# Optimization experiments

Measured on AMD Instinct MI355X. Metric: run time of the kernel, lower is better.

The kernel has to match this reference:

```python
import jax, jax.numpy as jnp
import numpy as np

E = 8        # n_routed_experts
Z = 4        # zero_expert_num (identity experts)
K = 2        # moe_topk
SCALE = 2.5  # routed_scaling_factor
T, H, I = 8192, 1024, 512


def setup_inputs() -> dict:
    key = jax.random.key(0)
    k0, k1, k2, k3, k4 = jax.random.split(key, 5)
    return {
        "hidden_states": jax.random.normal(k0, (T, H), jnp.float32),
        "router_w": jax.random.normal(k1, (E + Z, H), jnp.float32) * 0.02,
        "correction_bias": jax.random.normal(k2, (E + Z,), jnp.float32) * 0.01,
        "w13": jax.random.normal(k3, (E, 2 * I, H), jnp.float32) * 0.02,
        "w2": jax.random.normal(k4, (E, H, I), jnp.float32) * 0.02,
    }


def reference(hidden_states, router_w, correction_bias, w13, w2):
    # ---- router (float32) ----
    logits = hidden_states.astype(jnp.float32) @ router_w.T          # [T, E+Z]
    scores = jax.nn.softmax(logits, axis=-1)
    # correction bias only affects expert *selection*, not the gate weights
    _, topk_idx = jax.lax.top_k(scores + correction_bias, K)          # [T, K]
    topk_w = jnp.take_along_axis(scores, topk_idx, axis=-1)          # renormalize=False

    # ---- zero experts (identity type): idx >= E contributes scale * x ----
    is_zero = topk_idx >= E                                           # [T, K]
    routed_w = jnp.where(is_zero, 0.0, topk_w)
    zero_scale = jnp.where(is_zero, topk_w, 0.0).sum(-1, keepdims=True)
    zero_result = zero_scale * hidden_states                          # [T, H]

    # ---- combine weights per routed expert: [T, E] ----
    tok = jnp.arange(hidden_states.shape[0])[:, None]
    safe_idx = jnp.clip(topk_idx, 0, E - 1)   # zero-expert slots carry weight 0
    combine = jnp.zeros((hidden_states.shape[0], E), scores.dtype)
    combine = combine.at[tok, safe_idx].add(routed_w)

    # ---- grouped expert GEMMs (SiLU gated MLP), combined densely ----
    h = jnp.einsum('th,eih->eti', hidden_states, w13)                 # [E, T, 2I]
    g, u = jnp.split(h, 2, axis=-1)
    act = jax.nn.silu(g) * u                                          # [E, T, I]
    eo = jnp.einsum('eti,ehi->eth', act, w2)                          # [E, T, H]
    routed = jnp.einsum('te,eth->th', combine, eo)                    # [T, H]

    return routed * SCALE + zero_result
```

## Files before the change

kernel.cpp:

```cpp
#include <hip/hip_runtime.h>
#include <hip/hip_bf16.h>
#include <math.h>

typedef __bf16 bf16_t;
typedef bf16_t bf16x8 __attribute__((ext_vector_type(8)));
typedef float f32x4 __attribute__((ext_vector_type(4)));

#define T_TOK 8192
#define HDIM  1024
#define IDIM  512
#define NEXP  8
#define NTOT  12
#define MAXROWS (2 * T_TOK + NEXP * 128)
#define MAX_MTILES (MAXROWS / 128)

__device__ __forceinline__ void gll16(const bf16_t* g, bf16_t* l) {
  __builtin_amdgcn_global_load_lds((__attribute__((address_space(1))) void*)g,
                                   (__attribute__((address_space(3))) void*)l,
                                   16, 0, 0);
}

__global__ void cast_bf16_kernel(const float* __restrict__ in, bf16_t* __restrict__ out,
                                 size_t n8) {
  size_t gid = (size_t)blockIdx.x * blockDim.x + threadIdx.x;
  if (gid >= n8) return;
  size_t i = gid * 8;
  float4 a = *(const float4*)&in[i];
  float4 b = *(const float4*)&in[i + 4];
  bf16x8 o;
  o[0] = (bf16_t)a.x; o[1] = (bf16_t)a.y; o[2] = (bf16_t)a.z; o[3] = (bf16_t)a.w;
  o[4] = (bf16_t)b.x; o[5] = (bf16_t)b.y; o[6] = (bf16_t)b.z; o[7] = (bf16_t)b.w;
  *(bf16x8*)&out[i] = o;
}

__global__ void router_kernel(const float* __restrict__ x, const float* __restrict__ rw,
                              const float* __restrict__ bias,
                              int* __restrict__ tk_e, float* __restrict__ tk_w,
                              float* __restrict__ zscale) {
  int t = blockIdx.x;
  int l = threadIdx.x;
  const float4* xr = (const float4*)(x + (size_t)t * HDIM);
  float4 xv[4];
#pragma unroll
  for (int i = 0; i < 4; i++) xv[i] = xr[l + 64 * i];
  float part[NTOT];
#pragma unroll
  for (int e = 0; e < NTOT; e++) {
    const float4* wr = (const float4*)(rw + (size_t)e * HDIM);
    float s = 0.f;
#pragma unroll
    for (int i = 0; i < 4; i++) {
      float4 w = wr[l + 64 * i];
      s += xv[i].x * w.x + xv[i].y * w.y + xv[i].z * w.z + xv[i].w * w.w;
    }
    part[e] = s;
  }
#pragma unroll
  for (int off = 32; off > 0; off >>= 1)
#pragma unroll
    for (int e = 0; e < NTOT; e++) part[e] += __shfl_down(part[e], off);

  if (l == 0) {
    float mx = part[0];
#pragma unroll
    for (int e = 1; e < NTOT; e++) mx = fmaxf(mx, part[e]);
    float p[NTOT], den = 0.f;
#pragma unroll
    for (int e = 0; e < NTOT; e++) { p[e] = expf(part[e] - mx); den += p[e]; }
    float inv = 1.f / den;
#pragma unroll
    for (int e = 0; e < NTOT; e++) p[e] *= inv;
    float s0 = -1e30f, s1 = -1e30f; int i0 = 0, i1 = 0;
#pragma unroll
    for (int e = 0; e < NTOT; e++) {
      float v = p[e] + bias[e];
      if (v > s0) { s1 = s0; i1 = i0; s0 = v; i0 = e; }
      else if (v > s1) { s1 = v; i1 = e; }
    }
    float zs = 0.f;
    int idx[2] = { i0, i1 };
#pragma unroll
    for (int k = 0; k < 2; k++) {
      int e = idx[k];
      float w = p[e];
      if (e >= NEXP) { zs += w; tk_e[2 * t + k] = -1; tk_w[2 * t + k] = 0.f; }
      else           { tk_e[2 * t + k] = e; tk_w[2 * t + k] = w; }
    }
    zscale[t] = zs;
  }
}

__global__ void zero_init_kernel(int* __restrict__ counts, int* __restrict__ sel_tok,
                                 float* __restrict__ sel_w) {
  int i = blockIdx.x * blockDim.x + threadIdx.x;
  if (i < MAXROWS) { sel_tok[i] = 0; sel_w[i] = 0.f; }
  if (i < NEXP) counts[i] = 0;
}

__global__ void count_kernel(const int* __restrict__ tk_e, int* __restrict__ counts) {
  __shared__ int lc[NEXP];
  int tid = threadIdx.x;
  if (tid < NEXP) lc[tid] = 0;
  __syncthreads();
  int t = blockIdx.x * blockDim.x + tid;
  int e0 = tk_e[2 * t], e1 = tk_e[2 * t + 1];
  if (e0 >= 0) atomicAdd(&lc[e0], 1);
  if (e1 >= 0) atomicAdd(&lc[e1], 1);
  __syncthreads();
  if (tid < NEXP) atomicAdd(&counts[tid], lc[tid]);
}

__global__ void scan_kernel(const int* __restrict__ counts, int* __restrict__ off_pad,
                            int* __restrict__ cursor, int* __restrict__ total_rows,
                            int* __restrict__ tile_e, int* __restrict__ tile_p0,
                            int* __restrict__ n_mtiles) {
  if (threadIdx.x == 0) {
    int run = 0, nt = 0;
    for (int e = 0; e < NEXP; e++) {
      off_pad[e] = run;
      cursor[e] = run;
      int ntile = (counts[e] + 127) / 128;
      for (int i = 0; i < ntile; i++) {
        tile_e[nt] = e;
        tile_p0[nt] = run + i * 128;
        nt++;
      }
      run += ntile * 128;
    }
    *total_rows = run;
    *n_mtiles = nt;
  }
}

__global__ void assign_kernel(const int* __restrict__ tk_e, const float* __restrict__ tk_w,
                              int* __restrict__ cursor, int* __restrict__ sel_tok,
                              float* __restrict__ sel_w, int* __restrict__ pos) {
  __shared__ int lc[NEXP];
  __shared__ int lbase[NEXP];
  int tid = threadIdx.x;
  if (tid < NEXP) lc[tid] = 0;
  __syncthreads();
  int t = blockIdx.x * blockDim.x + tid;
  int e0 = tk_e[2 * t], e1 = tk_e[2 * t + 1];
  int r0 = (e0 >= 0) ? atomicAdd(&lc[e0], 1) : -1;
  int r1 = (e1 >= 0) ? atomicAdd(&lc[e1], 1) : -1;
  __syncthreads();
  if (tid < NEXP) lbase[tid] = atomicAdd(&cursor[tid], lc[tid]);
  __syncthreads();
  int p0 = -1, p1 = -1;
  if (e0 >= 0) { p0 = lbase[e0] + r0; sel_tok[p0] = t; sel_w[p0] = 2.5f * tk_w[2 * t]; }
  if (e1 >= 0) { p1 = lbase[e1] + r1; sel_tok[p1] = t; sel_w[p1] = 2.5f * tk_w[2 * t + 1]; }
  pos[2 * t] = p0;
  pos[2 * t + 1] = p1;
}

__global__ void gather_cast_kernel(const float* __restrict__ x, const int* __restrict__ sel_tok,
                                   const int* __restrict__ total_rows, bf16_t* __restrict__ xg) {
  size_t gid = (size_t)blockIdx.x * blockDim.x + threadIdx.x;
  size_t p = gid >> 7;
  if (p >= (size_t)*total_rows) return;
  size_t j = (gid & 127) << 3;
  int t = sel_tok[p];
  float4 a = *(const float4*)&x[(size_t)t * HDIM + j];
  float4 b = *(const float4*)&x[(size_t)t * HDIM + j + 4];
  bf16x8 o;
  o[0] = (bf16_t)a.x; o[1] = (bf16_t)a.y; o[2] = (bf16_t)a.z; o[3] = (bf16_t)a.w;
  o[4] = (bf16_t)b.x; o[5] = (bf16_t)b.y; o[6] = (bf16_t)b.z; o[7] = (bf16_t)b.w;
  *(bf16x8*)&xg[p * HDIM + j] = o;
}

__global__ __launch_bounds__(256) void gemm1_kernel(
    const bf16_t* __restrict__ xg, const bf16_t* __restrict__ w13b,
    const int* __restrict__ tile_e, const int* __restrict__ tile_p0,
    const int* __restrict__ n_mtiles, bf16_t* __restrict__ actb) {
  const int ti = blockIdx.x;
  if (ti >= *n_mtiles) return;
  const int e = tile_e[ti];
  const int p0 = tile_p0[ti];
  const int g0 = blockIdx.y * 64;

  __shared__ alignas(16) bf16_t As[128 * 32];
  __shared__ alignas(16) bf16_t Bs[128 * 32];
  const int tid = threadIdx.x;
  const int w = tid >> 6, l = tid & 63;
  const int wr = w >> 1, wc = w & 1;
  const int quad = l >> 4, c16 = l & 15;

  const int sr = w * 32 + (l >> 2);
  const int sc = (l & 3) * 8;
  const bf16_t* Ag0 = xg + (size_t)(p0 + sr) * HDIM + sc;
  const bf16_t* w13e = w13b + (size_t)e * (2 * IDIM) * HDIM;
  int r0 = sr, r1 = sr + 16;
  int col0 = g0 + (r0 >> 6) * 32 + (((r0 >> 4) & 1) * 16) + (r0 & 15) + (((r0 >> 5) & 1) ? IDIM : 0);
  int col1 = g0 + (r1 >> 6) * 32 + (((r1 >> 4) & 1) * 16) + (r1 & 15) + (((r1 >> 5) & 1) ? IDIM : 0);
  const bf16_t* Bg0 = w13e + (size_t)col0 * HDIM + sc;
  const bf16_t* Bg1 = w13e + (size_t)col1 * HDIM + sc;
  bf16_t* Al0 = &As[(w * 32) * 32];
  bf16_t* Bl0 = &Bs[(w * 32) * 32];

  f32x4 acc[4][4];
#pragma unroll
  for (int i = 0; i < 4; i++)
#pragma unroll
    for (int j = 0; j < 4; j++) acc[i][j] = (f32x4){0.f, 0.f, 0.f, 0.f};

  for (int k0 = 0; k0 < HDIM; k0 += 32) {
    gll16(Ag0 + k0, Al0);
    gll16(Ag0 + k0 + (size_t)16 * HDIM, Al0 + 16 * 32);
    gll16(Bg0 + k0, Bl0);
    gll16(Bg1 + k0, Bl0 + 16 * 32);
    __syncthreads();
    bf16x8 af[4], bfv[4];
#pragma unroll
    for (int mt = 0; mt < 4; mt++)
      af[mt] = *(const bf16x8*)&As[(wr * 64 + mt * 16 + c16) * 32 + quad * 8];
#pragma unroll
    for (int nt = 0; nt < 4; nt++)
      bfv[nt] = *(const bf16x8*)&Bs[(wc * 64 + nt * 16 + c16) * 32 + quad * 8];
#pragma unroll
    for (int mt = 0; mt < 4; mt++)
#pragma unroll
      for (int nt = 0; nt < 4; nt++)
        acc[mt][nt] = __builtin_amdgcn_mfma_f32_16x16x32_bf16(af[mt], bfv[nt], acc[mt][nt], 0, 0, 0);
    __syncthreads();
  }

#pragma unroll
  for (int mt = 0; mt < 4; mt++) {
    int rowb = p0 + wr * 64 + mt * 16 + quad * 4;
#pragma unroll
    for (int nt = 0; nt < 2; nt++) {
      int col = g0 + wc * 32 + nt * 16 + c16;
#pragma unroll
      for (int r = 0; r < 4; r++) {
        float g = acc[mt][nt][r];
        float u = acc[mt][nt + 2][r];
        float s = g / (1.f + expf(-g));
        actb[(size_t)(rowb + r) * IDIM + col] = (bf16_t)(s * u);
      }
    }
  }
}

__global__ __launch_bounds__(256) void gemm2_kernel(
    const bf16_t* __restrict__ actb, const bf16_t* __restrict__ w2b,
    const float* __restrict__ sel_w, const int* __restrict__ tile_e,
    const int* __restrict__ tile_p0, const int* __restrict__ n_mtiles,
    bf16_t* __restrict__ eob) {
  const int ti = blockIdx.x;
  if (ti >= *n_mtiles) return;
  const int e = tile_e[ti];
  const int p0 = tile_p0[ti];
  const int n0 = blockIdx.y * 128;

  __shared__ alignas(16) bf16_t As[128 * 32];
  __shared__ alignas(16) bf16_t Bs[128 * 32];
  const int tid = threadIdx.x;
  const int w = tid >> 6, l = tid & 63;
  const int wr = w >> 1, wc = w & 1;
  const int quad = l >> 4, c16 = l & 15;

  const int sr = w * 32 + (l >> 2);
  const int sc = (l & 3) * 8;
  const bf16_t* Ag0 = actb + (size_t)(p0 + sr) * IDIM + sc;
  const bf16_t* Bg0 = w2b + (size_t)e * HDIM * IDIM + (size_t)(n0 + sr) * IDIM + sc;
  bf16_t* Al0 = &As[(w * 32) * 32];
  bf16_t* Bl0 = &Bs[(w * 32) * 32];

  f32x4 acc[4][4];
#pragma unroll
  for (int i = 0; i < 4; i++)
#pragma unroll
    for (int j = 0; j < 4; j++) acc[i][j] = (f32x4){0.f, 0.f, 0.f, 0.f};

  for (int k0 = 0; k0 < IDIM; k0 += 32) {
    gll16(Ag0 + k0, Al0);
    gll16(Ag0 + k0 + (size_t)16 * IDIM, Al0 + 16 * 32);
    gll16(Bg0 + k0, Bl0);
    gll16(Bg0 + k0 + (size_t)16 * IDIM, Bl0 + 16 * 32);
    __syncthreads();
    bf16x8 af[4], bfv[4];
#pragma unroll
    for (int mt = 0; mt < 4; mt++)
      af[mt] = *(const bf16x8*)&As[(wr * 64 + mt * 16 + c16) * 32 + quad * 8];
#pragma unroll
    for (int nt = 0; nt < 4; nt++)
      bfv[nt] = *(const bf16x8*)&Bs[(wc * 64 + nt * 16 + c16) * 32 + quad * 8];
#pragma unroll
    for (int mt = 0; mt < 4; mt++)
#pragma unroll
      for (int nt = 0; nt < 4; nt++)
        acc[mt][nt] = __builtin_amdgcn_mfma_f32_16x16x32_bf16(af[mt], bfv[nt], acc[mt][nt], 0, 0, 0);
    __syncthreads();
  }

#pragma unroll
  for (int mt = 0; mt < 4; mt++) {
    int rowb = wr * 64 + mt * 16 + quad * 4;
    float cw[4];
#pragma unroll
    for (int r = 0; r < 4; r++) cw[r] = sel_w[p0 + rowb + r];
#pragma unroll
    for (int nt = 0; nt < 4; nt++) {
      int col = n0 + wc * 64 + nt * 16 + c16;
#pragma unroll
      for (int r = 0; r < 4; r++)
        eob[(size_t)(p0 + rowb + r) * HDIM + col] = (bf16_t)(cw[r] * acc[mt][nt][r]);
    }
  }
}

__global__ void combine_kernel(const float* __restrict__ x, const float* __restrict__ zscale,
                               const int* __restrict__ pos, const bf16_t* __restrict__ eob,
                               float* __restrict__ out) {
  size_t gid = (size_t)blockIdx.x * blockDim.x + threadIdx.x;
  size_t t = gid >> 7;
  size_t j = (gid & 127) << 3;
  float zs = zscale[t];
  int p0 = pos[2 * t], p1 = pos[2 * t + 1];
  float4 a = *(const float4*)&x[t * HDIM + j];
  float4 b = *(const float4*)&x[t * HDIM + j + 4];
  float o[8] = { zs * a.x, zs * a.y, zs * a.z, zs * a.w,
                 zs * b.x, zs * b.y, zs * b.z, zs * b.w };
  if (p0 >= 0) {
    bf16x8 v = *(const bf16x8*)&eob[(size_t)p0 * HDIM + j];
#pragma unroll
    for (int k = 0; k < 8; k++) o[k] += (float)v[k];
  }
  if (p1 >= 0) {
    bf16x8 v = *(const bf16x8*)&eob[(size_t)p1 * HDIM + j];
#pragma unroll
    for (int k = 0; k < 8; k++) o[k] += (float)v[k];
  }
  *(float4*)&out[t * HDIM + j] = make_float4(o[0], o[1], o[2], o[3]);
  *(float4*)&out[t * HDIM + j + 4] = make_float4(o[4], o[5], o[6], o[7]);
}

extern "C" void kernel_launch(void* const* d_in, const int* in_sizes, int n_in,
                              void* d_out, int out_size, void* d_ws, size_t ws_size,
                              hipStream_t stream) {
  const float* x    = (const float*)d_in[0];
  const float* rw   = (const float*)d_in[1];
  const float* bias = (const float*)d_in[2];
  const float* w13  = (const float*)d_in[3];
  const float* w2   = (const float*)d_in[4];
  float* out = (float*)d_out;

  char* ws = (char*)d_ws;
  bf16_t* w13b = (bf16_t*)ws;  ws += (size_t)NEXP * 2 * IDIM * HDIM * 2;
  bf16_t* w2b  = (bf16_t*)ws;  ws += (size_t)NEXP * HDIM * IDIM * 2;
  bf16_t* xg   = (bf16_t*)ws;  ws += (size_t)MAXROWS * HDIM * 2;
  bf16_t* actb = (bf16_t*)ws;  ws += (size_t)MAXROWS * IDIM * 2;
  bf16_t* eob  = (bf16_t*)ws;  ws += (size_t)MAXROWS * HDIM * 2;
  int*   tk_e    = (int*)ws;   ws += (size_t)T_TOK * 2 * 4;
  float* tk_w    = (float*)ws; ws += (size_t)T_TOK * 2 * 4;
  float* zscale  = (float*)ws; ws += (size_t)T_TOK * 4;
  int*   pos     = (int*)ws;   ws += (size_t)T_TOK * 2 * 4;
  int*   sel_tok = (int*)ws;   ws += (size_t)MAXROWS * 4;
  float* sel_w   = (float*)ws; ws += (size_t)MAXROWS * 4;
  int*   counts  = (int*)ws;   ws += NEXP * 4;
  int*   off_pad = (int*)ws;   ws += NEXP * 4;
  int*   cursor  = (int*)ws;   ws += NEXP * 4;
  int*   total_rows = (int*)ws; ws += 4;
  int*   tile_e  = (int*)ws;   ws += MAX_MTILES * 4;
  int*   tile_p0 = (int*)ws;   ws += MAX_MTILES * 4;
  int*   n_mtiles = (int*)ws;  ws += 4;

  {
    size_t n8 = (size_t)NEXP * 2 * IDIM * HDIM / 8;
    cast_bf16_kernel<<<(n8 + 255) / 256, 256, 0, stream>>>(w13, w13b, n8);
    n8 = (size_t)NEXP * HDIM * IDIM / 8;
    cast_bf16_kernel<<<(n8 + 255) / 256, 256, 0, stream>>>(w2, w2b, n8);
  }
  router_kernel<<<T_TOK, 64, 0, stream>>>(x, rw, bias, tk_e, tk_w, zscale);
  zero_init_kernel<<<(MAXROWS + 255) / 256, 256, 0, stream>>>(counts, sel_tok, sel_w);
  count_kernel<<<T_TOK / 256, 256, 0, stream>>>(tk_e, counts);
  scan_kernel<<<1, 64, 0, stream>>>(counts, off_pad, cursor, total_rows,
                                    tile_e, tile_p0, n_mtiles);
  assign_kernel<<<T_TOK / 256, 256, 0, stream>>>(tk_e, tk_w, cursor, sel_tok, sel_w, pos);
  gather_cast_kernel<<<(size_t)MAXROWS * (HDIM / 8) / 256, 256, 0, stream>>>(
      x, sel_tok, total_rows, xg);

  gemm1_kernel<<<dim3(MAX_MTILES, IDIM / 64), 256, 0, stream>>>(
      xg, w13b, tile_e, tile_p0, n_mtiles, actb);
  gemm2_kernel<<<dim3(MAX_MTILES, HDIM / 128), 256, 0, stream>>>(
      actb, w2b, sel_w, tile_e, tile_p0, n_mtiles, eob);

  combine_kernel<<<(size_t)T_TOK * HDIM / 8 / 256, 256, 0, stream>>>(
      x, zscale, pos, eob, out);
}
```

Before: 235.6 us.

## Fuse prep kernels, gather tokens inside GEMM1, widen K tile with swizzled LDS

Several independent changes land together. The two weight casts and the sel_tok/sel_w zeroing merge into one kernel, and the x-to-bf16 cast moves into the router. Count and scan become a single one-block kernel. The separate gather kernel is removed, and GEMM1 now reads token rows through sel_tok directly. Both GEMMs change from a K step of 32 to 64 with an XOR-swizzled LDS layout, which halves barrier count and reduces bank conflicts, at the cost of doubling LDS use.

New measurement: 247.3 us. 4.9% more time.

```diff
diff --git a/kernel.cpp b/kernel.cpp
--- a/kernel.cpp
+++ b/kernel.cpp
@@ -3,6 +3,7 @@
 #include <math.h>
 
 typedef __bf16 bf16_t;
+typedef bf16_t bf16x4 __attribute__((ext_vector_type(4)));
 typedef bf16_t bf16x8 __attribute__((ext_vector_type(8)));
 typedef float f32x4 __attribute__((ext_vector_type(4)));
 
@@ -20,11 +21,17 @@
                                    16, 0, 0);
 }
 
-__global__ void cast_bf16_kernel(const float* __restrict__ in, bf16_t* __restrict__ out,
-                                 size_t n8) {
+__global__ void wcast_init_kernel(const float* __restrict__ w13, const float* __restrict__ w2,
+                                  bf16_t* __restrict__ w13b, bf16_t* __restrict__ w2b,
+                                  int* __restrict__ sel_tok, float* __restrict__ sel_w) {
   size_t gid = (size_t)blockIdx.x * blockDim.x + threadIdx.x;
-  if (gid >= n8) return;
-  size_t i = gid * 8;
+  if (gid < MAXROWS) { sel_tok[gid] = 0; sel_w[gid] = 0.f; }
+  const size_t n13 = (size_t)NEXP * 2 * IDIM * HDIM / 8;
+  const size_t n2  = (size_t)NEXP * HDIM * IDIM / 8;
+  const float* in; bf16_t* out; size_t i;
+  if (gid < n13)            { in = w13; out = w13b; i = gid * 8; }
+  else if (gid < n13 + n2)  { in = w2;  out = w2b;  i = (gid - n13) * 8; }
+  else return;
   float4 a = *(const float4*)&in[i];
   float4 b = *(const float4*)&in[i + 4];
   bf16x8 o;
@@ -36,13 +43,20 @@
 __global__ void router_kernel(const float* __restrict__ x, const float* __restrict__ rw,
                               const float* __restrict__ bias,
                               int* __restrict__ tk_e, float* __restrict__ tk_w,
-                              float* __restrict__ zscale) {
+                              float* __restrict__ zscale, bf16_t* __restrict__ xb) {
   int t = blockIdx.x;
   int l = threadIdx.x;
   const float4* xr = (const float4*)(x + (size_t)t * HDIM);
   float4 xv[4];
 #pragma unroll
   for (int i = 0; i < 4; i++) xv[i] = xr[l + 64 * i];
+#pragma unroll
+  for (int i = 0; i < 4; i++) {
+    bf16x4 o;
+    o[0] = (bf16_t)xv[i].x; o[1] = (bf16_t)xv[i].y;
+    o[2] = (bf16_t)xv[i].z; o[3] = (bf16_t)xv[i].w;
+    *(bf16x4*)&xb[(size_t)t * HDIM + (size_t)(l + 64 * i) * 4] = o;
+  }
   float part[NTOT];
 #pragma unroll
   for (int e = 0; e < NTOT; e++) {
@@ -90,36 +104,34 @@
   }
 }
 
-__global__ void zero_init_kernel(int* __restrict__ counts, int* __restrict__ sel_tok,
-                                 float* __restrict__ sel_w) {
-  int i = blockIdx.x * blockDim.x + threadIdx.x;
-  if (i < MAXROWS) { sel_tok[i] = 0; sel_w[i] = 0.f; }
-  if (i < NEXP) counts[i] = 0;
-}
-
-__global__ void count_kernel(const int* __restrict__ tk_e, int* __restrict__ counts) {
+__global__ void countscan_kernel(const int* __restrict__ tk_e, int* __restrict__ cursor,
+                                 int* __restrict__ total_rows, int* __restrict__ tile_e,
+                                 int* __restrict__ tile_p0, int* __restrict__ n_mtiles) {
   __shared__ int lc[NEXP];
   int tid = threadIdx.x;
   if (tid < NEXP) lc[tid] = 0;
   __syncthreads();
-  int t = blockIdx.x * blockDim.x + tid;
-  int e0 = tk_e[2 * t], e1 = tk_e[2 * t + 1];
-  if (e0 >= 0) atomicAdd(&lc[e0], 1);
-  if (e1 >= 0) atomicAdd(&lc[e1], 1);
+  int cnt[NEXP];
+#pragma unroll
+  for (int j = 0; j < NEXP; j++) cnt[j] = 0;
+  for (int i = tid; i < 2 * T_TOK; i += 256) {
+    int e = tk_e[i];
+#pragma unroll
+    for (int j = 0; j < NEXP; j++) cnt[j] += (e == j) ? 1 : 0;
+  }
+#pragma unroll
+  for (int off = 32; off > 0; off >>= 1)
+#pragma unroll
+    for (int j = 0; j < NEXP; j++) cnt[j] += __shfl_down(cnt[j], off);
+  if ((tid & 63) == 0)
+#pragma unroll
+    for (int j = 0; j < NEXP; j++) atomicAdd(&lc[j], cnt[j]);
   __syncthreads();
-  if (tid < NEXP) atomicAdd(&counts[tid], lc[tid]);
-}
-
-__global__ void scan_kernel(const int* __restrict__ counts, int* __restrict__ off_pad,
-                            int* __restrict__ cursor, int* __restrict__ total_rows,
-                            int* __restrict__ tile_e, int* __restrict__ tile_p0,
-                            int* __restrict__ n_mtiles) {
-  if (threadIdx.x == 0) {
+  if (tid == 0) {
     int run = 0, nt = 0;
     for (int e = 0; e < NEXP; e++) {
-      off_pad[e] = run;
       cursor[e] = run;
-      int ntile = (counts[e] + 127) / 128;
+      int ntile = (lc[e] + 127) / 128;
       for (int i = 0; i < ntile; i++) {
         tile_e[nt] = e;
         tile_p0[nt] = run + i * 128;
@@ -154,49 +166,39 @@
   pos[2 * t + 1] = p1;
 }
 
-__global__ void gather_cast_kernel(const float* __restrict__ x, const int* __restrict__ sel_tok,
-                                   const int* __restrict__ total_rows, bf16_t* __restrict__ xg) {
-  size_t gid = (size_t)blockIdx.x * blockDim.x + threadIdx.x;
-  size_t p = gid >> 7;
-  if (p >= (size_t)*total_rows) return;
-  size_t j = (gid & 127) << 3;
-  int t = sel_tok[p];
-  float4 a = *(const float4*)&x[(size_t)t * HDIM + j];
-  float4 b = *(const float4*)&x[(size_t)t * HDIM + j + 4];
-  bf16x8 o;
-  o[0] = (bf16_t)a.x; o[1] = (bf16_t)a.y; o[2] = (bf16_t)a.z; o[3] = (bf16_t)a.w;
-  o[4] = (bf16_t)b.x; o[5] = (bf16_t)b.y; o[6] = (bf16_t)b.z; o[7] = (bf16_t)b.w;
-  *(bf16x8*)&xg[p * HDIM + j] = o;
-}
-
 __global__ __launch_bounds__(256) void gemm1_kernel(
-    const bf16_t* __restrict__ xg, const bf16_t* __restrict__ w13b,
-    const int* __restrict__ tile_e, const int* __restrict__ tile_p0,
-    const int* __restrict__ n_mtiles, bf16_t* __restrict__ actb) {
+    const bf16_t* __restrict__ xb, const bf16_t* __restrict__ w13b,
+    const int* __restrict__ sel_tok, const int* __restrict__ tile_e,
+    const int* __restrict__ tile_p0, const int* __restrict__ n_mtiles,
+    bf16_t* __restrict__ actb) {
   const int ti = blockIdx.x;
   if (ti >= *n_mtiles) return;
   const int e = tile_e[ti];
   const int p0 = tile_p0[ti];
   const int g0 = blockIdx.y * 64;
 
-  __shared__ alignas(16) bf16_t As[128 * 32];
-  __shared__ alignas(16) bf16_t Bs[128 * 32];
+  __shared__ alignas(16) bf16_t As[128 * 64];
+  __shared__ alignas(16) bf16_t Bs[128 * 64];
   const int tid = threadIdx.x;
   const int w = tid >> 6, l = tid & 63;
   const int wr = w >> 1, wc = w & 1;
   const int quad = l >> 4, c16 = l & 15;
 
-  const int sr = w * 32 + (l >> 2);
-  const int sc = (l & 3) * 8;
-  const bf16_t* Ag0 = xg + (size_t)(p0 + sr) * HDIM + sc;
+  const int lr = l >> 3;
+  const int csrc = ((l & 7) ^ lr) * 8;
   const bf16_t* w13e = w13b + (size_t)e * (2 * IDIM) * HDIM;
-  int r0 = sr, r1 = sr + 16;
-  int col0 = g0 + (r0 >> 6) * 32 + (((r0 >> 4) & 1) * 16) + (r0 & 15) + (((r0 >> 5) & 1) ? IDIM : 0);
-  int col1 = g0 + (r1 >> 6) * 32 + (((r1 >> 4) & 1) * 16) + (r1 & 15) + (((r1 >> 5) & 1) ? IDIM : 0);
-  const bf16_t* Bg0 = w13e + (size_t)col0 * HDIM + sc;
-  const bf16_t* Bg1 = w13e + (size_t)col1 * HDIM + sc;
-  bf16_t* Al0 = &As[(w * 32) * 32];
-  bf16_t* Bl0 = &Bs[(w * 32) * 32];
+  const bf16_t* Asrc[4];
+  const bf16_t* Bsrc[4];
+#pragma unroll
+  for (int s = 0; s < 4; s++) {
+    int r = w * 32 + s * 8 + lr;
+    int tok = sel_tok[p0 + r];
+    Asrc[s] = xb + (size_t)tok * HDIM + csrc;
+    int col = g0 + (r >> 6) * 32 + (((r >> 4) & 1) * 16) + (r & 15) + (((r >> 5) & 1) ? IDIM : 0);
+    Bsrc[s] = w13e + (size_t)col * HDIM + csrc;
+  }
+  bf16_t* Adst = &As[(w * 32) * 64];
+  bf16_t* Bdst = &Bs[(w * 32) * 64];
 
   f32x4 acc[4][4];
 #pragma unroll
@@ -204,24 +206,28 @@
 #pragma unroll
     for (int j = 0; j < 4; j++) acc[i][j] = (f32x4){0.f, 0.f, 0.f, 0.f};
 
-  for (int k0 = 0; k0 < HDIM; k0 += 32) {
-    gll16(Ag0 + k0, Al0);
-    gll16(Ag0 + k0 + (size_t)16 * HDIM, Al0 + 16 * 32);
-    gll16(Bg0 + k0, Bl0);
-    gll16(Bg1 + k0, Bl0 + 16 * 32);
+  for (int k0 = 0; k0 < HDIM; k0 += 64) {
+#pragma unroll
+    for (int s = 0; s < 4; s++) {
+      gll16(Asrc[s] + k0, Adst + s * 8 * 64);
+      gll16(Bsrc[s] + k0, Bdst + s * 8 * 64);
+    }
     __syncthreads();
-    bf16x8 af[4], bfv[4];
-#pragma unroll
-    for (int mt = 0; mt < 4; mt++)
-      af[mt] = *(const bf16x8*)&As[(wr * 64 + mt * 16 + c16) * 32 + quad * 8];
-#pragma unroll
-    for (int nt = 0; nt < 4; nt++)
-      bfv[nt] = *(const bf16x8*)&Bs[(wc * 64 + nt * 16 + c16) * 32 + quad * 8];
-#pragma unroll
-    for (int mt = 0; mt < 4; mt++)
+#pragma unroll
+    for (int kk = 0; kk < 2; kk++) {
+      bf16x8 af[4], bfv[4];
+#pragma unroll
+      for (int mt = 0; mt < 4; mt++)
+        af[mt] = *(const bf16x8*)&As[(wr * 64 + mt * 16 + c16) * 64 + (((kk * 4 + quad) ^ (c16 & 7)) * 8)];
 #pragma unroll
       for (int nt = 0; nt < 4; nt++)
-        acc[mt][nt] = __builtin_amdgcn_mfma_f32_16x16x32_bf16(af[mt], bfv[nt], acc[mt][nt], 0, 0, 0);
+        bfv[nt] = *(const bf16x8*)&Bs[(wc * 64 + nt * 16 + c16) * 64 + (((kk * 4 + quad) ^ (c16 & 7)) * 8)];
+#pragma unroll
+      for (int mt = 0; mt < 4; mt++)
+#pragma unroll
+        for (int nt = 0; nt < 4; nt++)
+          acc[mt][nt] = __builtin_amdgcn_mfma_f32_16x16x32_bf16(af[mt], bfv[nt], acc[mt][nt], 0, 0, 0);
+    }
     __syncthreads();
   }
 
@@ -253,19 +259,25 @@
   const int p0 = tile_p0[ti];
   const int n0 = blockIdx.y * 128;
 
-  __shared__ alignas(16) bf16_t As[128 * 32];
-  __shared__ alignas(16) bf16_t Bs[128 * 32];
+  __shared__ alignas(16) bf16_t As[128 * 64];
+  __shared__ alignas(16) bf16_t Bs[128 * 64];
   const int tid = threadIdx.x;
   const int w = tid >> 6, l = tid & 63;
   const int wr = w >> 1, wc = w & 1;
   const int quad = l >> 4, c16 = l & 15;
 
-  const int sr = w * 32 + (l >> 2);
-  const int sc = (l & 3) * 8;
-  const bf16_t* Ag0 = actb + (size_t)(p0 + sr) * IDIM + sc;
-  const bf16_t* Bg0 = w2b + (size_t)e * HDIM * IDIM + (size_t)(n0 + sr) * IDIM + sc;
-  bf16_t* Al0 = &As[(w * 32) * 32];
-  bf16_t* Bl0 = &Bs[(w * 32) * 32];
+  const int lr = l >> 3;
+  const int csrc = ((l & 7) ^ lr) * 8;
+  const bf16_t* Asrc[4];
+  const bf16_t* Bsrc[4];
+#pragma unroll
+  for (int s = 0; s < 4; s++) {
+    int r = w * 32 + s * 8 + lr;
+    Asrc[s] = actb + (size_t)(p0 + r) * IDIM + csrc;
+    Bsrc[s] = w2b + (size_t)e * HDIM * IDIM + (size_t)(n0 + r) * IDIM + csrc;
+  }
+  bf16_t* Adst = &As[(w * 32) * 64];
+  bf16_t* Bdst = &Bs[(w * 32) * 64];
 
   f32x4 acc[4][4];
 #pragma unroll
@@ -273,24 +285,28 @@
 #pragma unroll
     for (int j = 0; j < 4; j++) acc[i][j] = (f32x4){0.f, 0.f, 0.f, 0.f};
 
-  for (int k0 = 0; k0 < IDIM; k0 += 32) {
-    gll16(Ag0 + k0, Al0);
-    gll16(Ag0 + k0 + (size_t)16 * IDIM, Al0 + 16 * 32);
-    gll16(Bg0 + k0, Bl0);
-    gll16(Bg0 + k0 + (size_t)16 * IDIM, Bl0 + 16 * 32);
+  for (int k0 = 0; k0 < IDIM; k0 += 64) {
+#pragma unroll
+    for (int s = 0; s < 4; s++) {
+      gll16(Asrc[s] + k0, Adst + s * 8 * 64);
+      gll16(Bsrc[s] + k0, Bdst + s * 8 * 64);
+    }
     __syncthreads();
-    bf16x8 af[4], bfv[4];
-#pragma unroll
-    for (int mt = 0; mt < 4; mt++)
-      af[mt] = *(const bf16x8*)&As[(wr * 64 + mt * 16 + c16) * 32 + quad * 8];
-#pragma unroll
-    for (int nt = 0; nt < 4; nt++)
-      bfv[nt] = *(const bf16x8*)&Bs[(wc * 64 + nt * 16 + c16) * 32 + quad * 8];
-#pragma unroll
-    for (int mt = 0; mt < 4; mt++)
+#pragma unroll
+    for (int kk = 0; kk < 2; kk++) {
+      bf16x8 af[4], bfv[4];
+#pragma unroll
+      for (int mt = 0; mt < 4; mt++)
+        af[mt] = *(const bf16x8*)&As[(wr * 64 + mt * 16 + c16) * 64 + (((kk * 4 + quad) ^ (c16 & 7)) * 8)];
 #pragma unroll
       for (int nt = 0; nt < 4; nt++)
-        acc[mt][nt] = __builtin_amdgcn_mfma_f32_16x16x32_bf16(af[mt], bfv[nt], acc[mt][nt], 0, 0, 0);
+        bfv[nt] = *(const bf16x8*)&Bs[(wc * 64 + nt * 16 + c16) * 64 + (((kk * 4 + quad) ^ (c16 & 7)) * 8)];
+#pragma unroll
+      for (int mt = 0; mt < 4; mt++)
+#pragma unroll
+        for (int nt = 0; nt < 4; nt++)
+          acc[mt][nt] = __builtin_amdgcn_mfma_f32_16x16x32_bf16(af[mt], bfv[nt], acc[mt][nt], 0, 0, 0);
+    }
     __syncthreads();
   }
 
@@ -349,7 +365,7 @@
   char* ws = (char*)d_ws;
   bf16_t* w13b = (bf16_t*)ws;  ws += (size_t)NEXP * 2 * IDIM * HDIM * 2;
   bf16_t* w2b  = (bf16_t*)ws;  ws += (size_t)NEXP * HDIM * IDIM * 2;
-  bf16_t* xg   = (bf16_t*)ws;  ws += (size_t)MAXROWS * HDIM * 2;
+  bf16_t* xb   = (bf16_t*)ws;  ws += (size_t)T_TOK * HDIM * 2;
   bf16_t* actb = (bf16_t*)ws;  ws += (size_t)MAXROWS * IDIM * 2;
   bf16_t* eob  = (bf16_t*)ws;  ws += (size_t)MAXROWS * HDIM * 2;
   int*   tk_e    = (int*)ws;   ws += (size_t)T_TOK * 2 * 4;
@@ -358,8 +374,6 @@
   int*   pos     = (int*)ws;   ws += (size_t)T_TOK * 2 * 4;
   int*   sel_tok = (int*)ws;   ws += (size_t)MAXROWS * 4;
   float* sel_w   = (float*)ws; ws += (size_t)MAXROWS * 4;
-  int*   counts  = (int*)ws;   ws += NEXP * 4;
-  int*   off_pad = (int*)ws;   ws += NEXP * 4;
   int*   cursor  = (int*)ws;   ws += NEXP * 4;
   int*   total_rows = (int*)ws; ws += 4;
   int*   tile_e  = (int*)ws;   ws += MAX_MTILES * 4;
@@ -367,22 +381,17 @@
   int*   n_mtiles = (int*)ws;  ws += 4;
 
   {
-    size_t n8 = (size_t)NEXP * 2 * IDIM * HDIM / 8;
-    cast_bf16_kernel<<<(n8 + 255) / 256, 256, 0, stream>>>(w13, w13b, n8);
-    n8 = (size_t)NEXP * HDIM * IDIM / 8;
-    cast_bf16_kernel<<<(n8 + 255) / 256, 256, 0, stream>>>(w2, w2b, n8);
-  }
-  router_kernel<<<T_TOK, 64, 0, stream>>>(x, rw, bias, tk_e, tk_w, zscale);
-  zero_init_kernel<<<(MAXROWS + 255) / 256, 256, 0, stream>>>(counts, sel_tok, sel_w);
-  count_kernel<<<T_TOK / 256, 256, 0, stream>>>(tk_e, counts);
-  scan_kernel<<<1, 64, 0, stream>>>(counts, off_pad, cursor, total_rows,
-                                    tile_e, tile_p0, n_mtiles);
+    size_t n8 = (size_t)NEXP * 2 * IDIM * HDIM / 8 + (size_t)NEXP * HDIM * IDIM / 8;
+    wcast_init_kernel<<<(n8 + 255) / 256, 256, 0, stream>>>(w13, w2, w13b, w2b,
+                                                            sel_tok, sel_w);
+  }
+  router_kernel<<<T_TOK, 64, 0, stream>>>(x, rw, bias, tk_e, tk_w, zscale, xb);
+  countscan_kernel<<<1, 256, 0, stream>>>(tk_e, cursor, total_rows,
+                                          tile_e, tile_p0, n_mtiles);
   assign_kernel<<<T_TOK / 256, 256, 0, stream>>>(tk_e, tk_w, cursor, sel_tok, sel_w, pos);
-  gather_cast_kernel<<<(size_t)MAXROWS * (HDIM / 8) / 256, 256, 0, stream>>>(
-      x, sel_tok, total_rows, xg);
 
   gemm1_kernel<<<dim3(MAX_MTILES, IDIM / 64), 256, 0, stream>>>(
-      xg, w13b, tile_e, tile_p0, n_mtiles, actb);
+      xb, w13b, sel_tok, tile_e, tile_p0, n_mtiles, actb);
   gemm2_kernel<<<dim3(MAX_MTILES, HDIM / 128), 256, 0, stream>>>(
       actb, w2b, sel_w, tile_e, tile_p0, n_mtiles, eob);
 
```
